# Performance work log

Hardware: AMD Instinct MI355X
Metric: run time of the kernel (lower is better)

Reference implementation:

```python
import jax, jax.numpy as jnp
import numpy as np

B, T, D = 4, 2048, 1024
H = 4                      # fla GatedLinearAttention default num_heads
K = D; V = D               # expand_k = expand_v = 1
DK = K // H; DV = V // H   # 256 each
LOW = 16                   # gate_low_rank_dim default
GLN = 16.0                 # gate_logit_normalizer default


def _layernorm(x, w, b, eps=1e-5):
    mu = x.mean(-1, keepdims=True)
    xc = x - mu
    var = (xc * xc).mean(-1, keepdims=True)
    return xc * jax.lax.rsqrt(var + eps) * w + b


def _rmsnorm(x, w, eps=1e-5):
    ms = (x * x).mean(-1, keepdims=True)
    return x * jax.lax.rsqrt(ms + eps) * w


def _gla_scan(q, k, v, gk):
    # q,k,gk: [B,T,H,DK]; v: [B,T,H,DV]
    scale = DK ** -0.5
    qT = jnp.moveaxis(q * scale, 1, 0)  # [T,B,H,DK]
    kT = jnp.moveaxis(k, 1, 0)
    vT = jnp.moveaxis(v, 1, 0)
    gT = jnp.moveaxis(gk, 1, 0)

    def step(h, inp):
        qt, kt, vt, gt = inp  # [B,H,DK]/[B,H,DV]
        h = h * jnp.exp(gt)[..., None] + kt[..., :, None] * vt[..., None, :]
        o = jnp.einsum('bhk,bhkv->bhv', qt, h)
        return h, o

    h0 = jnp.zeros((q.shape[0], H, DK, DV), q.dtype)
    _, oT = jax.lax.scan(step, h0, (qT, kT, vT, gT))
    return jnp.moveaxis(oT, 0, 1)  # [B,T,H,DV]


def setup_inputs() -> dict:
    key = jax.random.key(0)
    ks = jax.random.split(key, 12)
    rn = lambda k, s: jax.random.normal(k, s, jnp.float32) * 0.02
    return {
        'x': jax.random.normal(ks[0], (B, T, D), jnp.float32),
        'ln1_w': jnp.ones((D,), jnp.float32), 'ln1_b': jnp.zeros((D,), jnp.float32),
        'Wq': rn(ks[1], (D, K)), 'Wk': rn(ks[2], (D, K)), 'Wv': rn(ks[3], (D, V)),
        'Wg': rn(ks[4], (D, V)),
        'Wgk1': rn(ks[5], (D, LOW)), 'Wgk2': rn(ks[6], (LOW, K)), 'bgk2': jnp.zeros((K,), jnp.float32),
        'rms_w': jnp.ones((DV,), jnp.float32),
        'Wo': rn(ks[7], (V, D)),
        'ln2_w': jnp.ones((D,), jnp.float32), 'ln2_b': jnp.zeros((D,), jnp.float32),
        'W1': rn(ks[8], (D, 3 * D)), 'b1': jnp.zeros((3 * D,), jnp.float32),
        'W2': rn(ks[9], (3 * D, D)), 'b2': jnp.zeros((D,), jnp.float32),
    }


def reference(x, ln1_w, ln1_b, Wq, Wk, Wv, Wg, Wgk1, Wgk2, bgk2, rms_w, Wo,
              ln2_w, ln2_b, W1, b1, W2, b2):
    b, t = x.shape[0], x.shape[1]
    xn = _layernorm(x, ln1_w, ln1_b)
    q = (xn @ Wq).reshape(b, t, H, DK)
    k = (xn @ Wk).reshape(b, t, H, DK)
    v = (xn @ Wv).reshape(b, t, H, DV)
    # low-rank forget gate: logsigmoid / gate_logit_normalizer
    gk = (jax.nn.log_sigmoid((xn @ Wgk1) @ Wgk2 + bgk2) / GLN).reshape(b, t, H, DK)
    o = _gla_scan(q, k, v, gk)                      # [B,T,H,DV]
    g = (xn @ Wg).reshape(b, t, H, DV)              # output gate
    o = _rmsnorm(o, rms_w) * (g * jax.nn.sigmoid(g))  # gated RMSNorm (swish gate)
    o = o.reshape(b, t, V) @ Wo
    x = x + o
    xn2 = _layernorm(x, ln2_w, ln2_b)
    h = jax.nn.leaky_relu(xn2 @ W1 + b1, 0.01)
    h = h * h                                        # LeakyReLU^2
    x = x + (h @ W2 + b2)
    return x
```

## Files before the change

### kernel.cpp

```cpp
#include <hip/hip_runtime.h>
#include <math.h>

#define BB 4
#define TT 2048
#define DD 1024
#define HH 4
#define DK 256
#define DV 256
#define RR 8192
#define CHK 64
#define NCHK 32
#define SS ((size_t)RR * DD)

typedef __bf16 bf16x8 __attribute__((ext_vector_type(8)));
typedef float f32x4 __attribute__((ext_vector_type(4)));

static __device__ inline unsigned short f2bf(float f) {
  unsigned int u = __float_as_uint(f);
  unsigned int r = (u + 0x7fffu + ((u >> 16) & 1u)) >> 16;
  return (unsigned short)r;
}
static __device__ inline float bf2f(unsigned short h) {
  return __uint_as_float(((unsigned int)h) << 16);
}

static __device__ __forceinline__ void gload16(const unsigned short* g,
                                               unsigned short* l) {
  __builtin_amdgcn_global_load_lds(
      (const __attribute__((address_space(1))) void*)g,
      (__attribute__((address_space(3))) void*)l, 16, 0, 0);
}

__global__ __launch_bounds__(256) void ln_kernel(const float* __restrict__ x,
                                                 const float* __restrict__ w,
                                                 const float* __restrict__ b,
                                                 unsigned short* __restrict__ yb) {
  int row = blockIdx.x;
  const float* xr = x + (size_t)row * DD;
  unsigned short* ybr = yb + (size_t)row * DD;
  int tid = threadIdx.x;

  float4 v = ((const float4*)xr)[tid];
  float s = v.x + v.y + v.z + v.w;
  float ss = v.x * v.x + v.y * v.y + v.z * v.z + v.w * v.w;
#pragma unroll
  for (int o = 32; o > 0; o >>= 1) {
    s += __shfl_down(s, o);
    ss += __shfl_down(ss, o);
  }
  __shared__ float ls[4], lss[4];
  int wid = tid >> 6;
  if ((tid & 63) == 0) { ls[wid] = s; lss[wid] = ss; }
  __syncthreads();
  float sum = ls[0] + ls[1] + ls[2] + ls[3];
  float sumsq = lss[0] + lss[1] + lss[2] + lss[3];
  float mu = sum * (1.0f / DD);
  float var = sumsq * (1.0f / DD) - mu * mu;
  float rs = rsqrtf(var + 1e-5f);

  float4 wv = ((const float4*)w)[tid];
  float4 bv = ((const float4*)b)[tid];
  ushort4 ob;
  ob.x = f2bf((v.x - mu) * rs * wv.x + bv.x);
  ob.y = f2bf((v.y - mu) * rs * wv.y + bv.y);
  ob.z = f2bf((v.z - mu) * rs * wv.z + bv.z);
  ob.w = f2bf((v.w - mu) * rs * wv.w + bv.w);
  ((ushort4*)ybr)[tid] = ob;
}

__global__ __launch_bounds__(256) void transpose_cast(const float* __restrict__ W,
                                                      unsigned short* __restrict__ Wt,
                                                      int K, int N) {
  __shared__ float t[32][33];
  int k0 = blockIdx.y * 32, n0 = blockIdx.x * 32;
  int tid = threadIdx.x;
  int tx = tid & 31, ty = tid >> 5;
#pragma unroll
  for (int i = 0; i < 4; ++i)
    t[ty + i * 8][tx] = W[(size_t)(k0 + ty + i * 8) * N + n0 + tx];
  __syncthreads();
#pragma unroll
  for (int i = 0; i < 4; ++i)
    Wt[(size_t)(n0 + ty + i * 8) * K + k0 + tx] = f2bf(t[tx][ty + i * 8]);
}

template <int EPI, int OUTBF>
__global__ __launch_bounds__(256) void gemm_bf16(
    const unsigned short* __restrict__ A,
    const unsigned short* __restrict__ Bt,
    const float* __restrict__ bias, const float* __restrict__ Res,
    void* __restrict__ Cv, int M, int N, int K) {
  __shared__ unsigned short As[2][128 * 64];
  __shared__ unsigned short Bs[2][128 * 64];
  int tid = threadIdx.x;
  int nwg = gridDim.x * gridDim.y;
  int wg = blockIdx.y * gridDim.x + blockIdx.x;
  int cpx = nwg >> 3;
  wg = (wg & 7) * cpx + (wg >> 3);
  int m0 = (wg / gridDim.x) * 128, n0 = (wg % gridDim.x) * 128;
  int lane = tid & 63;
  int w64 = tid & 192;
  int wid = tid >> 6;
  int wm = (wid >> 1) * 64, wn = (wid & 1) * 64;
  int fr = lane & 15, fq = lane >> 4;

  f32x4 acc[4][4] = {};

  auto STAGE = [&](int buf, int k0) {
#pragma unroll
    for (int j = 0; j < 4; ++j) {
      int gl = j * 256 + tid;
      int row = gl >> 3;
      int gs = (gl & 7) ^ (row & 7);
      gload16(&A[(size_t)(m0 + row) * K + k0 + gs * 8],
              &As[buf][(size_t)(j * 256 + w64) * 8]);
      gload16(&Bt[(size_t)(n0 + row) * K + k0 + gs * 8],
              &Bs[buf][(size_t)(j * 256 + w64) * 8]);
    }
  };

  STAGE(0, 0);
  asm volatile("s_waitcnt vmcnt(0)");
  __syncthreads();

  int cur = 0;
  for (int k0 = 0; k0 < K; k0 += 64) {
    if (k0 + 64 < K) STAGE(cur ^ 1, k0 + 64);

#pragma unroll
    for (int ph = 0; ph < 2; ++ph) {
      bf16x8 af[4], bv[4];
#pragma unroll
      for (int i = 0; i < 4; ++i) {
        int ra = wm + i * 16 + fr;
        af[i] = *(const bf16x8*)&As[cur][ra * 64 + (((ph * 4 + fq) ^ (ra & 7)) * 8)];
        int rb = wn + i * 16 + fr;
        bv[i] = *(const bf16x8*)&Bs[cur][rb * 64 + (((ph * 4 + fq) ^ (rb & 7)) * 8)];
      }
#pragma unroll
      for (int i = 0; i < 4; ++i)
#pragma unroll
        for (int jj = 0; jj < 4; ++jj)
          acc[i][jj] = __builtin_amdgcn_mfma_f32_16x16x32_bf16(af[i], bv[jj],
                                                               acc[i][jj], 0, 0, 0);
    }
    __syncthreads();
    cur ^= 1;
  }

  int col = lane & 15;
  int rbase = (lane >> 4) * 4;
#pragma unroll
  for (int i = 0; i < 4; ++i) {
#pragma unroll
    for (int j = 0; j < 4; ++j) {
      int n = n0 + wn + j * 16 + col;
      float bvv = (EPI == 2 || EPI == 4) ? bias[n] : 0.0f;
#pragma unroll
      for (int r = 0; r < 4; ++r) {
        int m = m0 + wm + i * 16 + rbase + r;
        float vv = acc[i][j][r] + bvv;
        if (EPI == 2) {
          float t = vv > 0.0f ? vv : 0.01f * vv;
          vv = t * t;
        }
        if (EPI == 3 || EPI == 4) vv += Res[(size_t)m * N + n];
        if (EPI == 5) {
          ((unsigned short*)Cv)[(size_t)(n >> 10) * SS + (size_t)m * 1024 +
                                (n & 1023)] = f2bf(vv);
        } else if (OUTBF) {
          ((unsigned short*)Cv)[(size_t)m * N + n] = f2bf(vv);
        } else {
          ((float*)Cv)[(size_t)m * N + n] = vv;
        }
      }
    }
  }
}

__global__ __launch_bounds__(256) void gk_kernel(const unsigned short* __restrict__ xn,
                                                 const float* __restrict__ Wgk1,
                                                 const float* __restrict__ Wgk2,
                                                 const float* __restrict__ bgk2,
                                                 unsigned short* __restrict__ gk) {
  int row = blockIdx.x;
  const unsigned short* xr = xn + (size_t)row * DD;
  int tid = threadIdx.x;

  float t16[16];
#pragma unroll
  for (int j = 0; j < 16; ++j) t16[j] = 0.0f;

#pragma unroll
  for (int dd = 0; dd < 4; ++dd) {
    int d = tid + dd * 256;
    float xv = bf2f(xr[d]);
    const float4* wrow = (const float4*)(Wgk1 + (size_t)d * 16);
#pragma unroll
    for (int q = 0; q < 4; ++q) {
      float4 wq = wrow[q];
      t16[q * 4 + 0] += xv * wq.x;
      t16[q * 4 + 1] += xv * wq.y;
      t16[q * 4 + 2] += xv * wq.z;
      t16[q * 4 + 3] += xv * wq.w;
    }
  }
#pragma unroll
  for (int j = 0; j < 16; ++j) {
    float s = t16[j];
#pragma unroll
    for (int o = 32; o > 0; o >>= 1) s += __shfl_down(s, o);
    t16[j] = s;
  }
  __shared__ float tmp[4][16];
  __shared__ float tf[16];
  int wid = tid >> 6;
  if ((tid & 63) == 0) {
#pragma unroll
    for (int j = 0; j < 16; ++j) tmp[wid][j] = t16[j];
  }
  __syncthreads();
  if (tid < 16) tf[tid] = tmp[0][tid] + tmp[1][tid] + tmp[2][tid] + tmp[3][tid];
  __syncthreads();

  float tl[16];
#pragma unroll
  for (int j = 0; j < 16; ++j) tl[j] = tf[j];

#pragma unroll
  for (int jj = 0; jj < 4; ++jj) {
    int n = tid * 4 + jj;
    float z = bgk2[n];
#pragma unroll
    for (int j = 0; j < 16; ++j) z += tl[j] * Wgk2[j * 1024 + n];
    float ls = fminf(z, 0.0f) - log1pf(expf(-fabsf(z)));
    gk[(size_t)row * 1024 + n] = f2bf(ls * (1.0f / 16.0f));
  }
}

__global__ __launch_bounds__(256) void gate_chunk(const unsigned short* __restrict__ gk,
                                                  unsigned short* __restrict__ q,
                                                  unsigned short* __restrict__ k,
                                                  float* __restrict__ ebC) {
  int bid = blockIdx.x;
  int c = bid & 31;
  int h = (bid >> 5) & 3;
  int b = bid >> 7;
  int tid = threadIdx.x;
  size_t base = ((size_t)b * TT + c * CHK) * 1024 + h * 256 + tid;

  const float scale = 0.0625f;
  float cum = 0.0f;
  for (int t = 0; t < CHK; ++t) {
    size_t a = base + (size_t)t * 1024;
    cum += bf2f(gk[a]);
    q[a] = f2bf(bf2f(q[a]) * expf(cum) * scale);
    k[a] = f2bf(bf2f(k[a]) * expf(-cum));
  }
  ebC[((b * 4 + h) * NCHK + c) * 256 + tid] = expf(cum);
}

template <int WITHE>
__global__ __launch_bounds__(256) void trans_kernel(const unsigned short* __restrict__ in,
                                                    const float* __restrict__ ebC,
                                                    unsigned short* __restrict__ outT) {
  __shared__ unsigned short T[64][68];
  int bid = blockIdx.x;
  int dkt = bid & 3;
  int ct = (bid >> 2) & 31;
  int bh = bid >> 7;
  int b = bh >> 2, h = bh & 3;
  int tid = threadIdx.x;
  int r = tid >> 4;
  int c4 = (tid & 15) * 4;
  size_t srcbase = ((size_t)b * TT + ct * 64) * 1024 + h * 256 + dkt * 64;
#pragma unroll
  for (int i = 0; i < 4; ++i)
    *(ushort4*)&T[r + i * 16][c4] =
        *(const ushort4*)&in[srcbase + (size_t)(r + i * 16) * 1024 + c4];
  __syncthreads();
  size_t outbase = (size_t)bh * 524288 + (size_t)(dkt * 64) * 2048 + ct * 64;
  const float* ep = ebC + ((size_t)bh * 32 + ct) * 256 + dkt * 64;
#pragma unroll
  for (int i = 0; i < 4; ++i) {
    int dkl = r + i * 16;
    float e = WITHE ? ep[dkl] : 1.0f;
    ushort4 o;
    o.x = f2bf(bf2f(T[c4 + 0][dkl]) * e);
    o.y = f2bf(bf2f(T[c4 + 1][dkl]) * e);
    o.z = f2bf(bf2f(T[c4 + 2][dkl]) * e);
    o.w = f2bf(bf2f(T[c4 + 3][dkl]) * e);
    *(ushort4*)&outT[outbase + (size_t)dkl * 2048 + c4] = o;
  }
}

__global__ __launch_bounds__(256) void u_gemm(const unsigned short* __restrict__ khatT,
                                              const unsigned short* __restrict__ vT,
                                              unsigned short* __restrict__ UT) {
  __shared__ unsigned short As[128 * 64];
  __shared__ unsigned short Bs[128 * 64];
  int tid = threadIdx.x;
  int bid = blockIdx.x;
  int tile = bid & 3;
  int bhc = bid >> 2;
  int bh = bhc >> 5, c = bhc & 31;
  int m0 = (tile >> 1) * 128, n0 = (tile & 1) * 128;
  const unsigned short* Ab = vT + (size_t)bh * 524288 + c * 64;
  const unsigned short* Bb = khatT + (size_t)bh * 524288 + c * 64;
  unsigned short* Cb = UT + (size_t)bhc * 65536;

  int lane = tid & 63;
  int w64 = tid & 192;
  int wid = tid >> 6;
  int wm = (wid >> 1) * 64, wn = (wid & 1) * 64;
  int fr = lane & 15, fq = lane >> 4;

  f32x4 acc[4][4] = {};

#pragma unroll
  for (int j = 0; j < 4; ++j) {
    int gl = j * 256 + tid;
    int row = gl >> 3;
    int gs = (gl & 7) ^ (row & 7);
    gload16(&Ab[(size_t)(m0 + row) * 2048 + gs * 8],
            &As[(size_t)(j * 256 + w64) * 8]);
    gload16(&Bb[(size_t)(n0 + row) * 2048 + gs * 8],
            &Bs[(size_t)(j * 256 + w64) * 8]);
  }
  __syncthreads();

#pragma unroll
  for (int ph = 0; ph < 2; ++ph) {
    bf16x8 af[4], bv[4];
#pragma unroll
    for (int i = 0; i < 4; ++i) {
      int ra = wm + i * 16 + fr;
      af[i] = *(const bf16x8*)&As[ra * 64 + (((ph * 4 + fq) ^ (ra & 7)) * 8)];
      int rb = wn + i * 16 + fr;
      bv[i] = *(const bf16x8*)&Bs[rb * 64 + (((ph * 4 + fq) ^ (rb & 7)) * 8)];
    }
#pragma unroll
    for (int i = 0; i < 4; ++i)
#pragma unroll
      for (int jj = 0; jj < 4; ++jj)
        acc[i][jj] = __builtin_amdgcn_mfma_f32_16x16x32_bf16(af[i], bv[jj],
                                                             acc[i][jj], 0, 0, 0);
  }

  int col = lane & 15;
  int rbase = (lane >> 4) * 4;
#pragma unroll
  for (int i = 0; i < 4; ++i)
#pragma unroll
    for (int j = 0; j < 4; ++j) {
      int n = n0 + wn + j * 16 + col;
#pragma unroll
      for (int r = 0; r < 4; ++r) {
        int m = m0 + wm + i * 16 + rbase + r;
        Cb[(size_t)m * 256 + n] = f2bf(acc[i][j][r]);
      }
    }
}

__global__ __launch_bounds__(256) void hscan(unsigned short* __restrict__ UH,
                                             const float* __restrict__ ebC) {
  int bid = blockIdx.x;
  int bh = bid >> 8, dv = bid & 255;
  int tid = threadIdx.x;
  size_t base = ((size_t)bh * NCHK) * 65536 + (size_t)dv * 256 + tid;
  const float* ebb = ebC + (size_t)bh * NCHK * 256;
  float h = 0.0f;
  for (int c = 0; c < NCHK; ++c) {
    size_t a = base + (size_t)c * 65536;
    float u = bf2f(UH[a]);
    UH[a] = f2bf(h);
    h = ebb[c * 256 + tid] * h + u;
  }
}

__global__ __launch_bounds__(256) void intra_mfma(
    const unsigned short* __restrict__ qt, const unsigned short* __restrict__ kt,
    const unsigned short* __restrict__ vT, float* __restrict__ o) {
  __shared__ unsigned short QK[2][64 * 264];
  __shared__ unsigned short Sb[64 * 64];
  unsigned short* Vs = &QK[0][0];

  int bid = blockIdx.x;
  int c = bid & 31;
  int bh = bid >> 5;
  int b = bh >> 2, h = bh & 3;
  size_t rowbase = ((size_t)b * TT + c * 64) * 1024 + h * 256;
  size_t vtbase = (size_t)bh * 524288 + c * 64;
  int tid = threadIdx.x;
  int lane = tid & 63;
  int w = tid >> 6;
  int fr = lane & 15, fq = lane >> 4;

#pragma unroll
  for (int i = 0; i < 8; ++i) {
    int g = tid + i * 256;
    int row = g >> 5, gc = g & 31;
    *(bf16x8*)&QK[0][row * 264 + gc * 8] =
        *(const bf16x8*)&qt[rowbase + (size_t)row * 1024 + gc * 8];
    *(bf16x8*)&QK[1][row * 264 + gc * 8] =
        *(const bf16x8*)&kt[rowbase + (size_t)row * 1024 + gc * 8];
  }
  __syncthreads();

  {
    f32x4 accs[4] = {};
#pragma unroll
    for (int ks = 0; ks < 8; ++ks) {
      bf16x8 af = *(const bf16x8*)&QK[0][(w * 16 + fr) * 264 + ks * 32 + fq * 8];
#pragma unroll
      for (int si = 0; si < 4; ++si) {
        bf16x8 bf_ = *(const bf16x8*)&QK[1][(si * 16 + fr) * 264 + ks * 32 + fq * 8];
        accs[si] = __builtin_amdgcn_mfma_f32_16x16x32_bf16(af, bf_, accs[si], 0, 0, 0);
      }
    }
#pragma unroll
    for (int si = 0; si < 4; ++si) {
#pragma unroll
      for (int r = 0; r < 4; ++r) {
        int t = w * 16 + fq * 4 + r;
        int s = si * 16 + fr;
        float val = (s <= t) ? accs[si][r] : 0.0f;
        int gS = s >> 3;
        Sb[t * 64 + ((gS ^ (t & 7)) * 8) + (s & 7)] = f2bf(val);
      }
    }
  }
  __syncthreads();

#pragma unroll
  for (int i = 0; i < 8; ++i) {
    int g = tid + i * 256;
    int dv = g >> 3, gc = g & 7;
    *(bf16x8*)&Vs[dv * 72 + gc * 8] =
        *(const bf16x8*)&vT[vtbase + (size_t)dv * 2048 + gc * 8];
  }
  __syncthreads();

  {
    int dv0 = w * 64;
    f32x4 acco[4][4] = {};
#pragma unroll
    for (int ks = 0; ks < 2; ++ks) {
      bf16x8 af[4], bv[4];
#pragma unroll
      for (int ti = 0; ti < 4; ++ti) {
        int t = ti * 16 + fr;
        af[ti] = *(const bf16x8*)&Sb[t * 64 + (((ks * 4 + fq) ^ (t & 7)) * 8)];
      }
#pragma unroll
      for (int nj = 0; nj < 4; ++nj)
        bv[nj] = *(const bf16x8*)&Vs[(dv0 + nj * 16 + fr) * 72 + ks * 32 + fq * 8];
#pragma unroll
      for (int ti = 0; ti < 4; ++ti)
#pragma unroll
        for (int nj = 0; nj < 4; ++nj)
          acco[ti][nj] = __builtin_amdgcn_mfma_f32_16x16x32_bf16(af[ti], bv[nj],
                                                                 acco[ti][nj], 0, 0, 0);
    }
#pragma unroll
    for (int ti = 0; ti < 4; ++ti)
#pragma unroll
      for (int nj = 0; nj < 4; ++nj)
#pragma unroll
        for (int r = 0; r < 4; ++r) {
          int t = ti * 16 + fq * 4 + r;
          int dv = dv0 + nj * 16 + fr;
          o[rowbase + (size_t)t * 1024 + dv] = acco[ti][nj][r];
        }
  }
}

__global__ __launch_bounds__(256) void inter_mfma(
    const unsigned short* __restrict__ qt, const unsigned short* __restrict__ HT,
    float* __restrict__ o) {
  __shared__ unsigned short Qs[64 * 264];
  __shared__ unsigned short Hs[256 * 72];
  int bid = blockIdx.x;
  int c = bid & 31;
  int bh = bid >> 5;
  int b = bh >> 2, h = bh & 3;
  size_t rowbase = ((size_t)b * TT + c * 64) * 1024 + h * 256;
  size_t htbase = ((size_t)(bh * 32 + c)) * 65536;
  int tid = threadIdx.x;
  int lane = tid & 63;
  int w = tid >> 6;
  int fr = lane & 15, fq = lane >> 4;
  int dv0 = w * 64;

#pragma unroll
  for (int i = 0; i < 8; ++i) {
    int g = tid + i * 256;
    int row = g >> 5, gc = g & 31;
    *(bf16x8*)&Qs[row * 264 + gc * 8] =
        *(const bf16x8*)&qt[rowbase + (size_t)row * 1024 + gc * 8];
  }

  f32x4 acc[4][4] = {};
  for (int k4 = 0; k4 < 4; ++k4) {
    __syncthreads();
#pragma unroll
    for (int i = 0; i < 8; ++i) {
      int g = tid + i * 256;
      int dv = g >> 3, gc = g & 7;
      *(bf16x8*)&Hs[dv * 72 + gc * 8] =
          *(const bf16x8*)&HT[htbase + (size_t)dv * 256 + k4 * 64 + gc * 8];
    }
    __syncthreads();
#pragma unroll
    for (int ks = 0; ks < 2; ++ks) {
      bf16x8 af[4], bv[4];
#pragma unroll
      for (int ti = 0; ti < 4; ++ti)
        af[ti] = *(const bf16x8*)&Qs[(ti * 16 + fr) * 264 + k4 * 64 + ks * 32 + fq * 8];
#pragma unroll
      for (int nj = 0; nj < 4; ++nj)
        bv[nj] = *(const bf16x8*)&Hs[(dv0 + nj * 16 + fr) * 72 + ks * 32 + fq * 8];
#pragma unroll
      for (int ti = 0; ti < 4; ++ti)
#pragma unroll
        for (int nj = 0; nj < 4; ++nj)
          acc[ti][nj] = __builtin_amdgcn_mfma_f32_16x16x32_bf16(af[ti], bv[nj],
                                                                acc[ti][nj], 0, 0, 0);
    }
  }

#pragma unroll
  for (int ti = 0; ti < 4; ++ti)
#pragma unroll
    for (int nj = 0; nj < 4; ++nj)
#pragma unroll
      for (int r = 0; r < 4; ++r) {
        int t = ti * 16 + fq * 4 + r;
        int dv = dv0 + nj * 16 + fr;
        size_t a = rowbase + (size_t)t * 1024 + dv;
        o[a] += acc[ti][nj][r];
      }
}

__global__ __launch_bounds__(256) void grms_kernel(const float* __restrict__ o,
                                                   const unsigned short* __restrict__ g,
                                                   const float* __restrict__ rw,
                                                   unsigned short* __restrict__ og) {
  size_t base = (size_t)blockIdx.x * 256;
  int tid = threadIdx.x;
  float ov = o[base + tid];
  float s = ov * ov;
#pragma unroll
  for (int off = 32; off > 0; off >>= 1) s += __shfl_down(s, off);
  __shared__ float red[4];
  int wid = tid >> 6;
  if ((tid & 63) == 0) red[wid] = s;
  __syncthreads();
  float ms = (red[0] + red[1] + red[2] + red[3]) * (1.0f / 256.0f);
  float gv = bf2f(g[base + tid]);
  float sw = gv / (1.0f + expf(-gv));
  og[base + tid] = f2bf(ov * rsqrtf(ms + 1e-5f) * rw[tid] * sw);
}

extern "C" void kernel_launch(void* const* d_in, const int* in_sizes, int n_in,
                              void* d_out, int out_size, void* d_ws,
                              size_t ws_size, hipStream_t stream) {
  const float* x = (const float*)d_in[0];
  const float* ln1_w = (const float*)d_in[1];
  const float* ln1_b = (const float*)d_in[2];
  const float* Wq = (const float*)d_in[3];
  const float* Wk = (const float*)d_in[4];
  const float* Wv = (const float*)d_in[5];
  const float* Wg = (const float*)d_in[6];
  const float* Wgk1 = (const float*)d_in[7];
  const float* Wgk2 = (const float*)d_in[8];
  const float* bgk2 = (const float*)d_in[9];
  const float* rms_w = (const float*)d_in[10];
  const float* Wo = (const float*)d_in[11];
  const float* ln2_w = (const float*)d_in[12];
  const float* ln2_b = (const float*)d_in[13];
  const float* W1 = (const float*)d_in[14];
  const float* b1 = (const float*)d_in[15];
  const float* W2 = (const float*)d_in[16];
  const float* b2 = (const float*)d_in[17];
  float* out = (float*)d_out;

  const size_t S = SS;
  unsigned short* actb = (unsigned short*)d_ws;
  unsigned short* qb = actb + S;
  unsigned short* kb = qb + S;
  unsigned short* vb = kb + S;
  unsigned short* gb = vb + S;
  unsigned short* gkb = gb + S;
  float* ofs = (float*)(gkb + S);
  unsigned short* UH = (unsigned short*)(ofs + S);
  float* ebC = (float*)(UH + 4 * S);
  unsigned short* Wqkvgt = (unsigned short*)(ebC + 131072);
  unsigned short* Wot = Wqkvgt + 4194304;
  unsigned short* W1t = Wot + 1048576;
  unsigned short* W2t = W1t + 3145728;
  unsigned short* khatT = gkb;
  unsigned short* vT = actb;
  float* x1 = (float*)kb;
  unsigned short* hb = UH;

  dim3 blk(256);

  transpose_cast<<<dim3(32, 32), blk, 0, stream>>>(Wq, Wqkvgt, 1024, 1024);
  transpose_cast<<<dim3(32, 32), blk, 0, stream>>>(Wk, Wqkvgt + 1048576, 1024, 1024);
  transpose_cast<<<dim3(32, 32), blk, 0, stream>>>(Wv, Wqkvgt + 2097152, 1024, 1024);
  transpose_cast<<<dim3(32, 32), blk, 0, stream>>>(Wg, Wqkvgt + 3145728, 1024, 1024);
  transpose_cast<<<dim3(32, 32), blk, 0, stream>>>(Wo, Wot, 1024, 1024);
  transpose_cast<<<dim3(96, 32), blk, 0, stream>>>(W1, W1t, 1024, 3072);
  transpose_cast<<<dim3(32, 96), blk, 0, stream>>>(W2, W2t, 3072, 1024);

  ln_kernel<<<RR, blk, 0, stream>>>(x, ln1_w, ln1_b, actb);

  dim3 g4096(4096 / 128, RR / 128);
  gemm_bf16<5, 1><<<g4096, blk, 0, stream>>>(actb, Wqkvgt, nullptr, nullptr, qb,
                                             RR, 4096, 1024);

  gk_kernel<<<RR, blk, 0, stream>>>(actb, Wgk1, Wgk2, bgk2, gkb);

  gate_chunk<<<BB * HH * NCHK, blk, 0, stream>>>(gkb, qb, kb, ebC);

  trans_kernel<1><<<16 * 32 * 4, blk, 0, stream>>>(kb, ebC, khatT);
  trans_kernel<0><<<16 * 32 * 4, blk, 0, stream>>>(vb, ebC, vT);

  u_gemm<<<16 * NCHK * 4, blk, 0, stream>>>(khatT, vT, UH);
  hscan<<<16 * 256, blk, 0, stream>>>(UH, ebC);

  intra_mfma<<<16 * NCHK, blk, 0, stream>>>(qb, kb, vT, ofs);
  inter_mfma<<<16 * NCHK, blk, 0, stream>>>(qb, UH, ofs);

  grms_kernel<<<RR * HH, blk, 0, stream>>>(ofs, gb, rms_w, actb);

  dim3 g1024(1024 / 128, RR / 128);
  gemm_bf16<3, 0><<<g1024, blk, 0, stream>>>(actb, Wot, nullptr, x, x1, RR, 1024, 1024);

  ln_kernel<<<RR, blk, 0, stream>>>(x1, ln2_w, ln2_b, actb);

  dim3 g3072(3072 / 128, RR / 128);
  gemm_bf16<2, 1><<<g3072, blk, 0, stream>>>(actb, W1t, b1, nullptr, hb, RR, 3072, 1024);

  gemm_bf16<4, 0><<<g1024, blk, 0, stream>>>(hb, W2t, b2, x1, out, RR, 1024, 3072);
}
```

Baseline: 474.4 us.

## Replace 128x128 bf16 GEMM with 256x256 tile, 512-thread, two-stage prefetch kernel

All four dense projections now use a 256x256 output tile per workgroup with 8 waves, each wave computing 128x64. Each shared-memory tile is reused by more MFMAs, cutting global and LDS traffic per flop. The loop prefetches two K-steps ahead with explicit vmcnt waits and raised wave priority around the MFMA bursts, so loads overlap compute. The cost is 128KB of LDS and more accumulator registers, which lowers occupancy. The 1024-wide GEMMs also drop to 128 workgroups, which may underfill the GPU's compute units.

```diff
diff --git a/kernel.cpp b/kernel.cpp
--- a/kernel.cpp
+++ b/kernel.cpp
@@ -85,73 +85,103 @@
 }
 
 template <int EPI, int OUTBF>
-__global__ __launch_bounds__(256) void gemm_bf16(
+__global__ __launch_bounds__(512) void gemm256(
     const unsigned short* __restrict__ A,
     const unsigned short* __restrict__ Bt,
     const float* __restrict__ bias, const float* __restrict__ Res,
     void* __restrict__ Cv, int M, int N, int K) {
-  __shared__ unsigned short As[2][128 * 64];
-  __shared__ unsigned short Bs[2][128 * 64];
+  __shared__ unsigned short As[2][256 * 64];
+  __shared__ unsigned short Bs[2][256 * 64];
   int tid = threadIdx.x;
   int nwg = gridDim.x * gridDim.y;
   int wg = blockIdx.y * gridDim.x + blockIdx.x;
   int cpx = nwg >> 3;
   wg = (wg & 7) * cpx + (wg >> 3);
-  int m0 = (wg / gridDim.x) * 128, n0 = (wg % gridDim.x) * 128;
+  int m0 = (wg / gridDim.x) * 256, n0 = (wg % gridDim.x) * 256;
   int lane = tid & 63;
-  int w64 = tid & 192;
+  int w64 = tid & 448;
   int wid = tid >> 6;
-  int wm = (wid >> 1) * 64, wn = (wid & 1) * 64;
+  int wm = (wid >> 2) * 128;
+  int wn = (wid & 3) * 64;
   int fr = lane & 15, fq = lane >> 4;
 
-  f32x4 acc[4][4] = {};
+  f32x4 acc[8][4] = {};
 
   auto STAGE = [&](int buf, int k0) {
 #pragma unroll
     for (int j = 0; j < 4; ++j) {
-      int gl = j * 256 + tid;
+      int gl = j * 512 + tid;
       int row = gl >> 3;
       int gs = (gl & 7) ^ (row & 7);
       gload16(&A[(size_t)(m0 + row) * K + k0 + gs * 8],
-              &As[buf][(size_t)(j * 256 + w64) * 8]);
+              &As[buf][(size_t)(j * 512 + w64) * 8]);
+    }
+#pragma unroll
+    for (int j = 0; j < 4; ++j) {
+      int gl = j * 512 + tid;
+      int row = gl >> 3;
+      int gs = (gl & 7) ^ (row & 7);
       gload16(&Bt[(size_t)(n0 + row) * K + k0 + gs * 8],
-              &Bs[buf][(size_t)(j * 256 + w64) * 8]);
+              &Bs[buf][(size_t)(j * 512 + w64) * 8]);
     }
   };
 
+  int nt = K >> 6;
+
   STAGE(0, 0);
-  asm volatile("s_waitcnt vmcnt(0)");
-  __syncthreads();
-
-  int cur = 0;
-  for (int k0 = 0; k0 < K; k0 += 64) {
-    if (k0 + 64 < K) STAGE(cur ^ 1, k0 + 64);
-
-#pragma unroll
-    for (int ph = 0; ph < 2; ++ph) {
-      bf16x8 af[4], bv[4];
-#pragma unroll
-      for (int i = 0; i < 4; ++i) {
+  STAGE(1, 64);
+  asm volatile("s_waitcnt vmcnt(8)" ::: "memory");
+  __builtin_amdgcn_sched_barrier(0);
+  __builtin_amdgcn_s_barrier();
+  __builtin_amdgcn_sched_barrier(0);
+
+  for (int t = 0; t < nt; ++t) {
+    int cur = t & 1;
+    const unsigned short* Ab = &As[cur][0];
+    const unsigned short* Bb = &Bs[cur][0];
+#pragma unroll
+    for (int ks = 0; ks < 2; ++ks) {
+      bf16x8 af[8], bv[4];
+#pragma unroll
+      for (int i = 0; i < 8; ++i) {
         int ra = wm + i * 16 + fr;
-        af[i] = *(const bf16x8*)&As[cur][ra * 64 + (((ph * 4 + fq) ^ (ra & 7)) * 8)];
-        int rb = wn + i * 16 + fr;
-        bv[i] = *(const bf16x8*)&Bs[cur][rb * 64 + (((ph * 4 + fq) ^ (rb & 7)) * 8)];
-      }
-#pragma unroll
-      for (int i = 0; i < 4; ++i)
-#pragma unroll
-        for (int jj = 0; jj < 4; ++jj)
-          acc[i][jj] = __builtin_amdgcn_mfma_f32_16x16x32_bf16(af[i], bv[jj],
-                                                               acc[i][jj], 0, 0, 0);
-    }
-    __syncthreads();
-    cur ^= 1;
+        af[i] = *(const bf16x8*)&Ab[ra * 64 + (((ks * 4 + fq) ^ (ra & 7)) * 8)];
+      }
+#pragma unroll
+      for (int j = 0; j < 4; ++j) {
+        int rb = wn + j * 16 + fr;
+        bv[j] = *(const bf16x8*)&Bb[rb * 64 + (((ks * 4 + fq) ^ (rb & 7)) * 8)];
+      }
+      __builtin_amdgcn_s_setprio(1);
+#pragma unroll
+      for (int i = 0; i < 8; ++i)
+#pragma unroll
+        for (int j = 0; j < 4; ++j)
+          acc[i][j] = __builtin_amdgcn_mfma_f32_16x16x32_bf16(af[i], bv[j],
+                                                              acc[i][j], 0, 0, 0);
+      __builtin_amdgcn_s_setprio(0);
+    }
+    __builtin_amdgcn_sched_barrier(0);
+    __builtin_amdgcn_s_barrier();
+    __builtin_amdgcn_sched_barrier(0);
+    if (t + 2 < nt) {
+      STAGE(cur, (t + 2) * 64);
+      asm volatile("s_waitcnt vmcnt(8)" ::: "memory");
+      __builtin_amdgcn_sched_barrier(0);
+      __builtin_amdgcn_s_barrier();
+      __builtin_amdgcn_sched_barrier(0);
+    } else if (t + 1 < nt) {
+      asm volatile("s_waitcnt vmcnt(0)" ::: "memory");
+      __builtin_amdgcn_sched_barrier(0);
+      __builtin_amdgcn_s_barrier();
+      __builtin_amdgcn_sched_barrier(0);
+    }
   }
 
   int col = lane & 15;
   int rbase = (lane >> 4) * 4;
 #pragma unroll
-  for (int i = 0; i < 4; ++i) {
+  for (int i = 0; i < 8; ++i) {
 #pragma unroll
     for (int j = 0; j < 4; ++j) {
       int n = n0 + wn + j * 16 + col;
@@ -161,8 +191,8 @@
         int m = m0 + wm + i * 16 + rbase + r;
         float vv = acc[i][j][r] + bvv;
         if (EPI == 2) {
-          float t = vv > 0.0f ? vv : 0.01f * vv;
-          vv = t * t;
+          float t2 = vv > 0.0f ? vv : 0.01f * vv;
+          vv = t2 * t2;
         }
         if (EPI == 3 || EPI == 4) vv += Res[(size_t)m * N + n];
         if (EPI == 5) {
@@ -605,6 +635,7 @@
   unsigned short* hb = UH;
 
   dim3 blk(256);
+  dim3 blk512(512);
 
   transpose_cast<<<dim3(32, 32), blk, 0, stream>>>(Wq, Wqkvgt, 1024, 1024);
   transpose_cast<<<dim3(32, 32), blk, 0, stream>>>(Wk, Wqkvgt + 1048576, 1024, 1024);
@@ -616,9 +647,9 @@
 
   ln_kernel<<<RR, blk, 0, stream>>>(x, ln1_w, ln1_b, actb);
 
-  dim3 g4096(4096 / 128, RR / 128);
-  gemm_bf16<5, 1><<<g4096, blk, 0, stream>>>(actb, Wqkvgt, nullptr, nullptr, qb,
-                                             RR, 4096, 1024);
+  dim3 g4096(4096 / 256, RR / 256);
+  gemm256<5, 1><<<g4096, blk512, 0, stream>>>(actb, Wqkvgt, nullptr, nullptr, qb,
+                                              RR, 4096, 1024);
 
   gk_kernel<<<RR, blk, 0, stream>>>(actb, Wgk1, Wgk2, bgk2, gkb);
 
@@ -635,13 +666,13 @@
 
   grms_kernel<<<RR * HH, blk, 0, stream>>>(ofs, gb, rms_w, actb);
 
-  dim3 g1024(1024 / 128, RR / 128);
-  gemm_bf16<3, 0><<<g1024, blk, 0, stream>>>(actb, Wot, nullptr, x, x1, RR, 1024, 1024);
+  dim3 g1024(1024 / 256, RR / 256);
+  gemm256<3, 0><<<g1024, blk512, 0, stream>>>(actb, Wot, nullptr, x, x1, RR, 1024, 1024);
 
   ln_kernel<<<RR, blk, 0, stream>>>(x1, ln2_w, ln2_b, actb);
 
-  dim3 g3072(3072 / 128, RR / 128);
-  gemm_bf16<2, 1><<<g3072, blk, 0, stream>>>(actb, W1t, b1, nullptr, hb, RR, 3072, 1024);
-
-  gemm_bf16<4, 0><<<g1024, blk, 0, stream>>>(hb, W2t, b2, x1, out, RR, 1024, 3072);
-}
+  dim3 g3072(3072 / 256, RR / 256);
+  gemm256<2, 1><<<g3072, blk512, 0, stream>>>(actb, W1t, b1, nullptr, hb, RR, 3072, 1024);
+
+  gemm256<4, 0><<<g1024, blk512, 0, stream>>>(hb, W2t, b2, x1, out, RR, 1024, 3072);
+}
```

New measurement: 533.6 us. +12.5%, slower.

## Fuse intra-chunk, inter-chunk attention and gated RMSNorm into one kernel

Applied to the files above, without the earlier changes.

Replaces the separate intra_mfma, inter_mfma and grms_kernel launches with a single attn_fused kernel. It keeps the output accumulator in registers across the intra-chunk and inter-chunk MFMA phases, then computes the per-row RMS with shuffles plus a small shared reduction and applies the swish gate directly. It writes bf16 output straight into a new buffer for the Wo GEMM. The aim is to drop the fp32 intermediate output write, its read-modify-write and its re-read, plus two launches. The cost is a longer kernel per block with higher register pressure and LDS reuse of one buffer for K, V and H.

```diff
diff --git a/kernel.cpp b/kernel.cpp
--- a/kernel.cpp
+++ b/kernel.cpp
@@ -378,12 +378,15 @@
   }
 }
 
-__global__ __launch_bounds__(256) void intra_mfma(
+__global__ __launch_bounds__(256) void attn_fused(
     const unsigned short* __restrict__ qt, const unsigned short* __restrict__ kt,
-    const unsigned short* __restrict__ vT, float* __restrict__ o) {
-  __shared__ unsigned short QK[2][64 * 264];
+    const unsigned short* __restrict__ vT, const unsigned short* __restrict__ HT,
+    const unsigned short* __restrict__ gp, const float* __restrict__ rw,
+    unsigned short* __restrict__ og) {
+  __shared__ unsigned short Qs[64 * 264];
+  __shared__ unsigned short KVH[256 * 72];
   __shared__ unsigned short Sb[64 * 64];
-  unsigned short* Vs = &QK[0][0];
+  __shared__ float red[64][4];
 
   int bid = blockIdx.x;
   int c = bid & 31;
@@ -391,6 +394,7 @@
   int b = bh >> 2, h = bh & 3;
   size_t rowbase = ((size_t)b * TT + c * 64) * 1024 + h * 256;
   size_t vtbase = (size_t)bh * 524288 + c * 64;
+  size_t htbase = ((size_t)(bh * 32 + c)) * 65536;
   int tid = threadIdx.x;
   int lane = tid & 63;
   int w = tid >> 6;
@@ -398,11 +402,11 @@
 
 #pragma unroll
   for (int i = 0; i < 8; ++i) {
-    int g = tid + i * 256;
-    int row = g >> 5, gc = g & 31;
-    *(bf16x8*)&QK[0][row * 264 + gc * 8] =
+    int gg = tid + i * 256;
+    int row = gg >> 5, gc = gg & 31;
+    *(bf16x8*)&Qs[row * 264 + gc * 8] =
         *(const bf16x8*)&qt[rowbase + (size_t)row * 1024 + gc * 8];
-    *(bf16x8*)&QK[1][row * 264 + gc * 8] =
+    *(bf16x8*)&KVH[row * 264 + gc * 8] =
         *(const bf16x8*)&kt[rowbase + (size_t)row * 1024 + gc * 8];
   }
   __syncthreads();
@@ -411,10 +415,10 @@
     f32x4 accs[4] = {};
 #pragma unroll
     for (int ks = 0; ks < 8; ++ks) {
-      bf16x8 af = *(const bf16x8*)&QK[0][(w * 16 + fr) * 264 + ks * 32 + fq * 8];
+      bf16x8 af = *(const bf16x8*)&Qs[(w * 16 + fr) * 264 + ks * 32 + fq * 8];
 #pragma unroll
       for (int si = 0; si < 4; ++si) {
-        bf16x8 bf_ = *(const bf16x8*)&QK[1][(si * 16 + fr) * 264 + ks * 32 + fq * 8];
+        bf16x8 bf_ = *(const bf16x8*)&KVH[(si * 16 + fr) * 264 + ks * 32 + fq * 8];
         accs[si] = __builtin_amdgcn_mfma_f32_16x16x32_bf16(af, bf_, accs[si], 0, 0, 0);
       }
     }
@@ -425,8 +429,7 @@
         int t = w * 16 + fq * 4 + r;
         int s = si * 16 + fr;
         float val = (s <= t) ? accs[si][r] : 0.0f;
-        int gS = s >> 3;
-        Sb[t * 64 + ((gS ^ (t & 7)) * 8) + (s & 7)] = f2bf(val);
+        Sb[t * 64 + (((s >> 3) ^ (t & 7)) * 8) + (s & 7)] = f2bf(val);
       }
     }
   }
@@ -434,92 +437,54 @@
 
 #pragma unroll
   for (int i = 0; i < 8; ++i) {
-    int g = tid + i * 256;
-    int dv = g >> 3, gc = g & 7;
-    *(bf16x8*)&Vs[dv * 72 + gc * 8] =
+    int gg = tid + i * 256;
+    int dv = gg >> 3, gc = gg & 7;
+    *(bf16x8*)&KVH[dv * 72 + gc * 8] =
         *(const bf16x8*)&vT[vtbase + (size_t)dv * 2048 + gc * 8];
   }
   __syncthreads();
 
-  {
-    int dv0 = w * 64;
-    f32x4 acco[4][4] = {};
+  int dv0 = w * 64;
+  f32x4 acc[4][4] = {};
+
+#pragma unroll
+  for (int ks = 0; ks < 2; ++ks) {
+    bf16x8 af[4], bv[4];
+#pragma unroll
+    for (int ti = 0; ti < 4; ++ti) {
+      int t = ti * 16 + fr;
+      af[ti] = *(const bf16x8*)&Sb[t * 64 + (((ks * 4 + fq) ^ (t & 7)) * 8)];
+    }
+#pragma unroll
+    for (int nj = 0; nj < 4; ++nj)
+      bv[nj] = *(const bf16x8*)&KVH[(dv0 + nj * 16 + fr) * 72 + ks * 32 + fq * 8];
+#pragma unroll
+    for (int ti = 0; ti < 4; ++ti)
+#pragma unroll
+      for (int nj = 0; nj < 4; ++nj)
+        acc[ti][nj] = __builtin_amdgcn_mfma_f32_16x16x32_bf16(af[ti], bv[nj],
+                                                              acc[ti][nj], 0, 0, 0);
+  }
+
+  for (int k4 = 0; k4 < 4; ++k4) {
+    __syncthreads();
+#pragma unroll
+    for (int i = 0; i < 8; ++i) {
+      int gg = tid + i * 256;
+      int dv = gg >> 3, gc = gg & 7;
+      *(bf16x8*)&KVH[dv * 72 + gc * 8] =
+          *(const bf16x8*)&HT[htbase + (size_t)dv * 256 + k4 * 64 + gc * 8];
+    }
+    __syncthreads();
 #pragma unroll
     for (int ks = 0; ks < 2; ++ks) {
       bf16x8 af[4], bv[4];
 #pragma unroll
-      for (int ti = 0; ti < 4; ++ti) {
-        int t = ti * 16 + fr;
-        af[ti] = *(const bf16x8*)&Sb[t * 64 + (((ks * 4 + fq) ^ (t & 7)) * 8)];
-      }
-#pragma unroll
-      for (int nj = 0; nj < 4; ++nj)
-        bv[nj] = *(const bf16x8*)&Vs[(dv0 + nj * 16 + fr) * 72 + ks * 32 + fq * 8];
-#pragma unroll
-      for (int ti = 0; ti < 4; ++ti)
-#pragma unroll
-        for (int nj = 0; nj < 4; ++nj)
-          acco[ti][nj] = __builtin_amdgcn_mfma_f32_16x16x32_bf16(af[ti], bv[nj],
-                                                                 acco[ti][nj], 0, 0, 0);
-    }
-#pragma unroll
-    for (int ti = 0; ti < 4; ++ti)
-#pragma unroll
-      for (int nj = 0; nj < 4; ++nj)
-#pragma unroll
-        for (int r = 0; r < 4; ++r) {
-          int t = ti * 16 + fq * 4 + r;
-          int dv = dv0 + nj * 16 + fr;
-          o[rowbase + (size_t)t * 1024 + dv] = acco[ti][nj][r];
-        }
-  }
-}
-
-__global__ __launch_bounds__(256) void inter_mfma(
-    const unsigned short* __restrict__ qt, const unsigned short* __restrict__ HT,
-    float* __restrict__ o) {
-  __shared__ unsigned short Qs[64 * 264];
-  __shared__ unsigned short Hs[256 * 72];
-  int bid = blockIdx.x;
-  int c = bid & 31;
-  int bh = bid >> 5;
-  int b = bh >> 2, h = bh & 3;
-  size_t rowbase = ((size_t)b * TT + c * 64) * 1024 + h * 256;
-  size_t htbase = ((size_t)(bh * 32 + c)) * 65536;
-  int tid = threadIdx.x;
-  int lane = tid & 63;
-  int w = tid >> 6;
-  int fr = lane & 15, fq = lane >> 4;
-  int dv0 = w * 64;
-
-#pragma unroll
-  for (int i = 0; i < 8; ++i) {
-    int g = tid + i * 256;
-    int row = g >> 5, gc = g & 31;
-    *(bf16x8*)&Qs[row * 264 + gc * 8] =
-        *(const bf16x8*)&qt[rowbase + (size_t)row * 1024 + gc * 8];
-  }
-
-  f32x4 acc[4][4] = {};
-  for (int k4 = 0; k4 < 4; ++k4) {
-    __syncthreads();
-#pragma unroll
-    for (int i = 0; i < 8; ++i) {
-      int g = tid + i * 256;
-      int dv = g >> 3, gc = g & 7;
-      *(bf16x8*)&Hs[dv * 72 + gc * 8] =
-          *(const bf16x8*)&HT[htbase + (size_t)dv * 256 + k4 * 64 + gc * 8];
-    }
-    __syncthreads();
-#pragma unroll
-    for (int ks = 0; ks < 2; ++ks) {
-      bf16x8 af[4], bv[4];
-#pragma unroll
       for (int ti = 0; ti < 4; ++ti)
         af[ti] = *(const bf16x8*)&Qs[(ti * 16 + fr) * 264 + k4 * 64 + ks * 32 + fq * 8];
 #pragma unroll
       for (int nj = 0; nj < 4; ++nj)
-        bv[nj] = *(const bf16x8*)&Hs[(dv0 + nj * 16 + fr) * 72 + ks * 32 + fq * 8];
+        bv[nj] = *(const bf16x8*)&KVH[(dv0 + nj * 16 + fr) * 72 + ks * 32 + fq * 8];
 #pragma unroll
       for (int ti = 0; ti < 4; ++ti)
 #pragma unroll
@@ -529,37 +494,57 @@
     }
   }
 
-#pragma unroll
-  for (int ti = 0; ti < 4; ++ti)
-#pragma unroll
-    for (int nj = 0; nj < 4; ++nj)
+  float rstd[4][4];
+#pragma unroll
+  for (int ti = 0; ti < 4; ++ti) {
+#pragma unroll
+    for (int r = 0; r < 4; ++r) {
+      float s = 0.0f;
+#pragma unroll
+      for (int nj = 0; nj < 4; ++nj) {
+        float v = acc[ti][nj][r];
+        s += v * v;
+      }
+      s += __shfl_xor(s, 1);
+      s += __shfl_xor(s, 2);
+      s += __shfl_xor(s, 4);
+      s += __shfl_xor(s, 8);
+      rstd[ti][r] = s;
+    }
+  }
+  if (fr == 0) {
+#pragma unroll
+    for (int ti = 0; ti < 4; ++ti)
+#pragma unroll
+      for (int r = 0; r < 4; ++r)
+        red[ti * 16 + fq * 4 + r][w] = rstd[ti][r];
+  }
+  __syncthreads();
+#pragma unroll
+  for (int ti = 0; ti < 4; ++ti) {
+#pragma unroll
+    for (int r = 0; r < 4; ++r) {
+      int t = ti * 16 + fq * 4 + r;
+      float tot = red[t][0] + red[t][1] + red[t][2] + red[t][3];
+      rstd[ti][r] = rsqrtf(tot * (1.0f / 256.0f) + 1e-5f);
+    }
+  }
+#pragma unroll
+  for (int ti = 0; ti < 4; ++ti) {
+#pragma unroll
+    for (int nj = 0; nj < 4; ++nj) {
+      int dv = dv0 + nj * 16 + fr;
+      float rwv = rw[dv];
 #pragma unroll
       for (int r = 0; r < 4; ++r) {
         int t = ti * 16 + fq * 4 + r;
-        int dv = dv0 + nj * 16 + fr;
-        size_t a = rowbase + (size_t)t * 1024 + dv;
-        o[a] += acc[ti][nj][r];
+        float gv = bf2f(gp[rowbase + (size_t)t * 1024 + dv]);
+        float sw = gv / (1.0f + expf(-gv));
+        og[rowbase + (size_t)t * 1024 + dv] =
+            f2bf(acc[ti][nj][r] * rstd[ti][r] * rwv * sw);
       }
-}
-
-__global__ __launch_bounds__(256) void grms_kernel(const float* __restrict__ o,
-                                                   const unsigned short* __restrict__ g,
-                                                   const float* __restrict__ rw,
-                                                   unsigned short* __restrict__ og) {
-  size_t base = (size_t)blockIdx.x * 256;
-  int tid = threadIdx.x;
-  float ov = o[base + tid];
-  float s = ov * ov;
-#pragma unroll
-  for (int off = 32; off > 0; off >>= 1) s += __shfl_down(s, off);
-  __shared__ float red[4];
-  int wid = tid >> 6;
-  if ((tid & 63) == 0) red[wid] = s;
-  __syncthreads();
-  float ms = (red[0] + red[1] + red[2] + red[3]) * (1.0f / 256.0f);
-  float gv = bf2f(g[base + tid]);
-  float sw = gv / (1.0f + expf(-gv));
-  og[base + tid] = f2bf(ov * rsqrtf(ms + 1e-5f) * rw[tid] * sw);
+    }
+  }
 }
 
 extern "C" void kernel_launch(void* const* d_in, const int* in_sizes, int n_in,
@@ -592,8 +577,8 @@
   unsigned short* vb = kb + S;
   unsigned short* gb = vb + S;
   unsigned short* gkb = gb + S;
-  float* ofs = (float*)(gkb + S);
-  unsigned short* UH = (unsigned short*)(ofs + S);
+  unsigned short* ogb = gkb + S;
+  unsigned short* UH = ogb + 2 * S;
   float* ebC = (float*)(UH + 4 * S);
   unsigned short* Wqkvgt = (unsigned short*)(ebC + 131072);
   unsigned short* Wot = Wqkvgt + 4194304;
@@ -630,13 +615,10 @@
   u_gemm<<<16 * NCHK * 4, blk, 0, stream>>>(khatT, vT, UH);
   hscan<<<16 * 256, blk, 0, stream>>>(UH, ebC);
 
-  intra_mfma<<<16 * NCHK, blk, 0, stream>>>(qb, kb, vT, ofs);
-  inter_mfma<<<16 * NCHK, blk, 0, stream>>>(qb, UH, ofs);
-
-  grms_kernel<<<RR * HH, blk, 0, stream>>>(ofs, gb, rms_w, actb);
+  attn_fused<<<16 * NCHK, blk, 0, stream>>>(qb, kb, vT, UH, gb, rms_w, ogb);
 
   dim3 g1024(1024 / 128, RR / 128);
-  gemm_bf16<3, 0><<<g1024, blk, 0, stream>>>(actb, Wot, nullptr, x, x1, RR, 1024, 1024);
+  gemm_bf16<3, 0><<<g1024, blk, 0, stream>>>(ogb, Wot, nullptr, x, x1, RR, 1024, 1024);
 
   ln_kernel<<<RR, blk, 0, stream>>>(x1, ln2_w, ln2_b, actb);
 
```

Measured after the change: 445.2 us. 1.07x faster.
